# Kernel tuning notes

Hardware: AMD Instinct MI355X
Metric: run time of the kernel (lower is better)

Reference implementation:

```python
import jax, jax.numpy as jnp
import numpy as np

EPS = 1e-5

def conv2x2(x, w, b):
    # x: NCHW, w: OIHW (2x2), stride 2, valid padding
    y = jax.lax.conv_general_dilated(x, w, window_strides=(2, 2), padding='VALID',
                                     dimension_numbers=('NCHW', 'OIHW', 'NCHW'))
    return y + b[None, :, None, None]

def instancenorm(x):
    # per-sample, per-channel norm over H,W; biased variance, no affine (PyTorch defaults)
    mu = jnp.mean(x, axis=(2, 3), keepdims=True)
    var = jnp.mean(jnp.square(x - mu), axis=(2, 3), keepdims=True)
    return (x - mu) * jax.lax.rsqrt(var + EPS)

def lrelu(x):
    return jax.nn.leaky_relu(x, negative_slope=0.01)

def setup_inputs() -> dict:
    key = jax.random.key(0)
    ks = jax.random.split(key, 14)
    B, L = 256, 20
    s = 0.05
    inp = {
        'x': jax.random.normal(ks[0], (B, 3, 128, 128), jnp.float32),
        'labels': jax.random.uniform(ks[1], (B, L), jnp.float32),
        'w1': jax.random.normal(ks[2], (16, 3, 2, 2), jnp.float32) * s,
        'b1': jnp.zeros((16,), jnp.float32),
        'w2': jax.random.normal(ks[3], (32, 16 + L, 2, 2), jnp.float32) * s,
        'b2': jnp.zeros((32,), jnp.float32),
        'w3': jax.random.normal(ks[4], (64, 32, 2, 2), jnp.float32) * s,
        'b3': jnp.zeros((64,), jnp.float32),
        'w4': jax.random.normal(ks[5], (128, 64, 2, 2), jnp.float32) * s,
        'b4': jnp.zeros((128,), jnp.float32),
        'fcw1': jax.random.normal(ks[6], (1024, 128 * 8 * 8), jnp.float32) * s,
        'fcb1': jnp.zeros((1024,), jnp.float32),
        'fcw2': jax.random.normal(ks[7], (1, 1024), jnp.float32) * s,
        'fcb2': jnp.zeros((1,), jnp.float32),
    }
    return inp

def reference(x, labels, w1, b1, w2, b2, w3, b3, w4, b4, fcw1, fcb1, fcw2, fcb2):
    h = lrelu(instancenorm(conv2x2(x, w1, b1)))            # [B,16,64,64]
    # vectorized replacement of the per-element label broadcast loop
    lab = jnp.broadcast_to(labels[:, :, None, None],
                           (h.shape[0], labels.shape[1], h.shape[2], h.shape[3]))
    h = jnp.concatenate([h, lab], axis=1)                  # [B,36,64,64]
    h = lrelu(instancenorm(conv2x2(h, w2, b2)))            # [B,32,32,32]
    h = lrelu(instancenorm(conv2x2(h, w3, b3)))            # [B,64,16,16]
    h = lrelu(instancenorm(conv2x2(h, w4, b4)))            # [B,128,8,8]
    h = h.reshape(h.shape[0], -1)                          # [B,8192]
    h = lrelu(h @ fcw1.T + fcb1)                           # [B,1024]
    return h @ fcw2.T + fcb2                               # [B,1]
```

## Files before the change

kernel.cpp:

```cpp
#include <hip/hip_runtime.h>

#define EPSI 1e-5f

typedef __attribute__((ext_vector_type(8))) short bf16x8;
typedef __attribute__((ext_vector_type(4))) float f32x4;

__device__ __forceinline__ float lrelu(float x) { return x > 0.f ? x : 0.01f * x; }

__device__ __forceinline__ unsigned short f2bf(float x) {
    unsigned int u = __float_as_uint(x);
    return (unsigned short)((u + 0x7fffu + ((u >> 16) & 1u)) >> 16);
}
__device__ __forceinline__ float bflo(unsigned int v) { return __uint_as_float(v << 16); }
__device__ __forceinline__ float bfhi(unsigned int v) { return __uint_as_float(v & 0xFFFF0000u); }
__device__ __forceinline__ unsigned int pack2(float a, float b) {
    return (unsigned int)f2bf(a) | ((unsigned int)f2bf(b) << 16);
}
__device__ __forceinline__ bf16x8 pack8(float4 a, float4 b) {
    union { unsigned short u[8]; bf16x8 v; } p;
    p.u[0] = f2bf(a.x); p.u[1] = f2bf(a.y); p.u[2] = f2bf(a.z); p.u[3] = f2bf(a.w);
    p.u[4] = f2bf(b.x); p.u[5] = f2bf(b.y); p.u[6] = f2bf(b.z); p.u[7] = f2bf(b.w);
    return p.v;
}

__device__ __forceinline__ float2 block_reduce_sum2(float a, float b) {
    #pragma unroll
    for (int off = 1; off < 64; off <<= 1) {
        a += __shfl_xor(a, off, 64);
        b += __shfl_xor(b, off, 64);
    }
    __shared__ float lds[8];
    const int t = threadIdx.x;
    if ((t & 63) == 0) { lds[2 * (t >> 6)] = a; lds[2 * (t >> 6) + 1] = b; }
    __syncthreads();
    a = lds[0] + lds[2] + lds[4] + lds[6];
    b = lds[1] + lds[3] + lds[5] + lds[7];
    return make_float2(a, b);
}


__global__ __launch_bounds__(1024) void wprep(const float* __restrict__ w2,
                                              const float* __restrict__ w3,
                                              const float* __restrict__ w4,
                                              unsigned short* __restrict__ wk) {
    const int g = blockIdx.x * 1024 + threadIdx.x;
    if (g < 2048) {
        const int co = g >> 6, k = g & 63;
        const int ic = (k >> 4) * 4 + (k & 3), row = (k >> 3) & 1, tx = (k >> 2) & 1;
        wk[g] = f2bf(w2[co * 144 + ic * 4 + row * 2 + tx]);
    } else if (g < 10240) {
        const int e = g - 2048, co = e >> 7, k = e & 127;
        const int ic = (k >> 4) * 4 + (k & 3), row = (k >> 3) & 1, tx = (k >> 2) & 1;
        wk[g] = f2bf(w3[co * 128 + ic * 4 + row * 2 + tx]);
    } else if (g < 43008) {
        const int e = g - 10240, co = e >> 8, k = e & 255;
        const int ic = (k >> 4) * 4 + (k & 3), row = (k >> 3) & 1, tx = (k >> 2) & 1;
        wk[g] = f2bf(w4[co * 256 + ic * 4 + row * 2 + tx]);
    }
}

__global__ __launch_bounds__(1024, 1) void k1234(const float* __restrict__ x,
                                                 const float* __restrict__ w1,
                                                 const unsigned short* __restrict__ wk,
                                                 unsigned short* __restrict__ h4) {
    const int n = blockIdx.x;
    const int t = threadIdx.x;
    const int w = t >> 6, l = t & 63;
    __shared__ __align__(16) unsigned char smem[131072];
    __shared__ float red[16][64][2];
    __shared__ float msc[64][2];
    unsigned short* h1s = (unsigned short*)smem;
    unsigned short* h2s = (unsigned short*)smem;
    unsigned short* h3s = (unsigned short*)(smem + 65536);
    float* ps = (float*)smem;

    {
        const float* xn = x + (size_t)n * 49152;
        float acc[16][4];
        #pragma unroll
        for (int j = 0; j < 16; ++j)
            #pragma unroll
            for (int q = 0; q < 4; ++q) acc[j][q] = 0.f;
        #pragma unroll 1
        for (int ic = 0; ic < 3; ++ic) {
            const float* p = xn + ic * 16384;
            float2 v0[4], v1[4];
            #pragma unroll
            for (int q = 0; q < 4; ++q) {
                const int idx = t + 1024 * q;
                const int oy = idx >> 6, ox = idx & 63;
                v0[q] = ((const float2*)(p + (2 * oy) * 128))[ox];
                v1[q] = ((const float2*)(p + (2 * oy + 1) * 128))[ox];
            }
            #pragma unroll
            for (int j = 0; j < 16; ++j) {
                const float4 wv = *(const float4*)(w1 + j * 12 + ic * 4);
                #pragma unroll
                for (int q = 0; q < 4; ++q)
                    acc[j][q] += v0[q].x * wv.x + v0[q].y * wv.y + v1[q].x * wv.z + v1[q].y * wv.w;
            }
        }
        #pragma unroll
        for (int j = 0; j < 16; ++j) {
            float s1 = acc[j][0] + acc[j][1] + acc[j][2] + acc[j][3];
            float s2 = acc[j][0] * acc[j][0] + acc[j][1] * acc[j][1] +
                       acc[j][2] * acc[j][2] + acc[j][3] * acc[j][3];
            #pragma unroll
            for (int off = 1; off < 64; off <<= 1) {
                s1 += __shfl_xor(s1, off, 64);
                s2 += __shfl_xor(s2, off, 64);
            }
            if (l == 0) { red[w][j][0] = s1; red[w][j][1] = s2; }
        }
        __syncthreads();
        if (t < 16) {
            float s1 = 0.f, s2 = 0.f;
            #pragma unroll
            for (int ww = 0; ww < 16; ++ww) { s1 += red[ww][t][0]; s2 += red[ww][t][1]; }
            const float mean = s1 * (1.f / 4096.f);
            const float var = s2 * (1.f / 4096.f) - mean * mean;
            msc[t][0] = mean; msc[t][1] = rsqrtf(var + EPSI);
        }
        __syncthreads();
        #pragma unroll
        for (int q = 0; q < 4; ++q) {
            const int px = t + 1024 * q;
            #pragma unroll
            for (int q4 = 0; q4 < 4; ++q4) {
                const float n0 = lrelu((acc[4 * q4 + 0][q] - msc[4 * q4 + 0][0]) * msc[4 * q4 + 0][1]);
                const float n1 = lrelu((acc[4 * q4 + 1][q] - msc[4 * q4 + 1][0]) * msc[4 * q4 + 1][1]);
                const float n2 = lrelu((acc[4 * q4 + 2][q] - msc[4 * q4 + 2][0]) * msc[4 * q4 + 2][1]);
                const float n3 = lrelu((acc[4 * q4 + 3][q] - msc[4 * q4 + 3][0]) * msc[4 * q4 + 3][1]);
                uint2 u; u.x = pack2(n0, n1); u.y = pack2(n2, n3);
                *(uint2*)(&h1s[((size_t)q4 * 4096 + px) * 4]) = u;
            }
        }
    }
    __syncthreads();

    {
        const unsigned short* wk2 = wk;
        bf16x8 af[2][2];
        #pragma unroll
        for (int cf = 0; cf < 2; ++cf)
            #pragma unroll
            for (int ks = 0; ks < 2; ++ks)
                af[cf][ks] = *(const bf16x8*)(wk2 + (cf * 16 + (l & 15)) * 64 + ks * 32 + (l >> 4) * 8);
        f32x4 acc[4][2];
        const f32x4 z = {0.f, 0.f, 0.f, 0.f};
        #pragma unroll
        for (int pg = 0; pg < 4; ++pg) { acc[pg][0] = z; acc[pg][1] = z; }
        const int row = (l >> 4) & 1, icq0 = (l >> 4) >> 1;
        #pragma unroll
        for (int pg = 0; pg < 4; ++pg) {
            const int oy = 2 * w + (pg >> 1);
            const int ox = (pg & 1) * 16 + (l & 15);
            #pragma unroll
            for (int ks = 0; ks < 2; ++ks) {
                const bf16x8 bv = *(const bf16x8*)(&h1s[(ks * 2 + icq0) * 16384 + (2 * oy + row) * 256 + ox * 8]);
                acc[pg][0] = __builtin_amdgcn_mfma_f32_16x16x32_bf16(af[0][ks], bv, acc[pg][0], 0, 0, 0);
                acc[pg][1] = __builtin_amdgcn_mfma_f32_16x16x32_bf16(af[1][ks], bv, acc[pg][1], 0, 0, 0);
            }
        }
        #pragma unroll
        for (int cf = 0; cf < 2; ++cf) {
            #pragma unroll
            for (int r = 0; r < 4; ++r) {
                float s1 = acc[0][cf][r] + acc[1][cf][r] + acc[2][cf][r] + acc[3][cf][r];
                float s2 = acc[0][cf][r] * acc[0][cf][r] + acc[1][cf][r] * acc[1][cf][r] +
                           acc[2][cf][r] * acc[2][cf][r] + acc[3][cf][r] * acc[3][cf][r];
                #pragma unroll
                for (int off = 1; off < 16; off <<= 1) {
                    s1 += __shfl_xor(s1, off, 64);
                    s2 += __shfl_xor(s2, off, 64);
                }
                if ((l & 15) == 0) {
                    red[w][cf * 16 + (l >> 4) * 4 + r][0] = s1;
                    red[w][cf * 16 + (l >> 4) * 4 + r][1] = s2;
                }
            }
        }
        __syncthreads();
        if (t < 32) {
            float s1 = 0.f, s2 = 0.f;
            #pragma unroll
            for (int ww = 0; ww < 16; ++ww) { s1 += red[ww][t][0]; s2 += red[ww][t][1]; }
            const float mean = s1 * (1.f / 1024.f);
            const float var = s2 * (1.f / 1024.f) - mean * mean;
            msc[t][0] = mean; msc[t][1] = rsqrtf(var + EPSI);
        }
        __syncthreads();
        #pragma unroll
        for (int pg = 0; pg < 4; ++pg) {
            const int px = w * 64 + pg * 16 + (l & 15);
            #pragma unroll
            for (int cf = 0; cf < 2; ++cf) {
                const int co0 = cf * 16 + (l >> 4) * 4;
                float v[4];
                #pragma unroll
                for (int r = 0; r < 4; ++r)
                    v[r] = lrelu((acc[pg][cf][r] - msc[co0 + r][0]) * msc[co0 + r][1]);
                uint2 u; u.x = pack2(v[0], v[1]); u.y = pack2(v[2], v[3]);
                *(uint2*)(&h2s[((cf * 4 + (l >> 4)) * 1024 + px) * 4]) = u;
            }
        }
    }
    __syncthreads();

    {
        const unsigned short* wk3 = wk + 2048;
        f32x4 acc[4];
        const f32x4 z = {0.f, 0.f, 0.f, 0.f};
        #pragma unroll
        for (int cf = 0; cf < 4; ++cf) acc[cf] = z;
        const int row = (l >> 4) & 1, icq0 = (l >> 4) >> 1;
        #pragma unroll
        for (int ks = 0; ks < 4; ++ks) {
            const bf16x8 bv = *(const bf16x8*)(&h2s[(ks * 2 + icq0) * 4096 + (2 * w + row) * 128 + (l & 15) * 8]);
            #pragma unroll
            for (int cf = 0; cf < 4; ++cf) {
                const bf16x8 af = *(const bf16x8*)(wk3 + (cf * 16 + (l & 15)) * 128 + ks * 32 + (l >> 4) * 8);
                acc[cf] = __builtin_amdgcn_mfma_f32_16x16x32_bf16(af, bv, acc[cf], 0, 0, 0);
            }
        }
        #pragma unroll
        for (int cf = 0; cf < 4; ++cf) {
            #pragma unroll
            for (int r = 0; r < 4; ++r) {
                float s1 = acc[cf][r], s2 = acc[cf][r] * acc[cf][r];
                #pragma unroll
                for (int off = 1; off < 16; off <<= 1) {
                    s1 += __shfl_xor(s1, off, 64);
                    s2 += __shfl_xor(s2, off, 64);
                }
                if ((l & 15) == 0) {
                    red[w][cf * 16 + (l >> 4) * 4 + r][0] = s1;
                    red[w][cf * 16 + (l >> 4) * 4 + r][1] = s2;
                }
            }
        }
        __syncthreads();
        if (t < 64) {
            float s1 = 0.f, s2 = 0.f;
            #pragma unroll
            for (int ww = 0; ww < 16; ++ww) { s1 += red[ww][t][0]; s2 += red[ww][t][1]; }
            const float mean = s1 * (1.f / 256.f);
            const float var = s2 * (1.f / 256.f) - mean * mean;
            msc[t][0] = mean; msc[t][1] = rsqrtf(var + EPSI);
        }
        __syncthreads();
        const int px = w * 16 + (l & 15);
        #pragma unroll
        for (int cf = 0; cf < 4; ++cf) {
            const int co0 = cf * 16 + (l >> 4) * 4;
            float v[4];
            #pragma unroll
            for (int r = 0; r < 4; ++r)
                v[r] = lrelu((acc[cf][r] - msc[co0 + r][0]) * msc[co0 + r][1]);
            uint2 u; u.x = pack2(v[0], v[1]); u.y = pack2(v[2], v[3]);
            *(uint2*)(&h3s[((cf * 4 + (l >> 4)) * 256 + px) * 4]) = u;
        }
    }
    __syncthreads();

    {
        const unsigned short* wk4 = wk + 10240;
        const int cfp = w & 3, khalf = (w >> 2) & 1;
        f32x4 acc[4][2];
        const f32x4 z = {0.f, 0.f, 0.f, 0.f};
        #pragma unroll
        for (int pg = 0; pg < 4; ++pg) { acc[pg][0] = z; acc[pg][1] = z; }
        const int row = (l >> 4) & 1, icq0 = (l >> 4) >> 1;
        const int oyb = (l & 15) >> 3, ox = l & 7;
        if (w < 8) {
            #pragma unroll
            for (int ksl = 0; ksl < 4; ++ksl) {
                const int ks = khalf * 4 + ksl;
                bf16x8 af0 = *(const bf16x8*)(wk4 + ((cfp * 2 + 0) * 16 + (l & 15)) * 256 + ks * 32 + (l >> 4) * 8);
                bf16x8 af1 = *(const bf16x8*)(wk4 + ((cfp * 2 + 1) * 16 + (l & 15)) * 256 + ks * 32 + (l >> 4) * 8);
                #pragma unroll
                for (int pg = 0; pg < 4; ++pg) {
                    const int oy = pg * 2 + oyb;
                    const bf16x8 bv = *(const bf16x8*)(&h3s[(ks * 2 + icq0) * 1024 + (2 * oy + row) * 64 + ox * 8]);
                    acc[pg][0] = __builtin_amdgcn_mfma_f32_16x16x32_bf16(af0, bv, acc[pg][0], 0, 0, 0);
                    acc[pg][1] = __builtin_amdgcn_mfma_f32_16x16x32_bf16(af1, bv, acc[pg][1], 0, 0, 0);
                }
            }
        }
        if (w < 4) {
            #pragma unroll
            for (int pg = 0; pg < 4; ++pg)
                #pragma unroll
                for (int cfi = 0; cfi < 2; ++cfi)
                    #pragma unroll
                    for (int r = 0; r < 4; ++r)
                        ps[(cfp * 64 + l) * 32 + pg * 8 + cfi * 4 + r] = acc[pg][cfi][r];
        }
        __syncthreads();
        if (w >= 4 && w < 8) {
            unsigned short* on = h4 + (size_t)n * 8192;
            #pragma unroll
            for (int cfi = 0; cfi < 2; ++cfi) {
                #pragma unroll
                for (int r = 0; r < 4; ++r) {
                    float v[4];
                    #pragma unroll
                    for (int pg = 0; pg < 4; ++pg)
                        v[pg] = acc[pg][cfi][r] + ps[(cfp * 64 + l) * 32 + pg * 8 + cfi * 4 + r];
                    float s1 = v[0] + v[1] + v[2] + v[3];
                    float s2 = v[0] * v[0] + v[1] * v[1] + v[2] * v[2] + v[3] * v[3];
                    #pragma unroll
                    for (int off = 1; off < 16; off <<= 1) {
                        s1 += __shfl_xor(s1, off, 64);
                        s2 += __shfl_xor(s2, off, 64);
                    }
                    const float mean = s1 * (1.f / 64.f);
                    const float var = s2 * (1.f / 64.f) - mean * mean;
                    const float sc = rsqrtf(var + EPSI);
                    const int co = (cfp * 2 + cfi) * 16 + (l >> 4) * 4 + r;
                    #pragma unroll
                    for (int pg = 0; pg < 4; ++pg)
                        on[co * 64 + pg * 16 + (l & 15)] = f2bf(lrelu((v[pg] - mean) * sc));
                }
            }
        }
    }
}

__global__ __launch_bounds__(256, 2) void k5_fc1(const unsigned short* __restrict__ A,
                                                 const float* __restrict__ Wf,
                                                 unsigned short* __restrict__ Cp) {
    __shared__ unsigned short As[128 * 72];
    __shared__ unsigned short Bs[128 * 72];
    const int t = threadIdx.x;
    const int sk = blockIdx.x >> 4;
    const int tile = blockIdx.x & 15;
    const int mt = tile >> 3, nt = tile & 7;
    const int m0 = mt * 128, n0 = nt * 128;
    const int w = t >> 6, l = t & 63;
    const int wm = (w >> 1) * 64, wn = (w & 1) * 64;
    const int lr16 = l & 15, lk8 = (l >> 4) * 8;
    const int srow = t >> 3, scol = (t & 7) * 8;
    f32x4 acc[4][4];
    const f32x4 z = {0.f, 0.f, 0.f, 0.f};
    #pragma unroll
    for (int f = 0; f < 4; ++f)
        #pragma unroll
        for (int g = 0; g < 4; ++g) acc[f][g] = z;
    const int kbeg = sk * 256;
    #pragma unroll 1
    for (int kt = 0; kt < 4; ++kt) {
        const int kc = kbeg + kt * 64;
        bf16x8 av[4], bv[4];
        #pragma unroll
        for (int i = 0; i < 4; ++i) {
            av[i] = *(const bf16x8*)(A + (size_t)(m0 + srow + 32 * i) * 8192 + kc + scol);
            const float4 w0 = *(const float4*)(Wf + (size_t)(n0 + srow + 32 * i) * 8192 + kc + scol);
            const float4 w1 = *(const float4*)(Wf + (size_t)(n0 + srow + 32 * i) * 8192 + kc + scol + 4);
            bv[i] = pack8(w0, w1);
        }
        __syncthreads();
        #pragma unroll
        for (int i = 0; i < 4; ++i) {
            *(bf16x8*)&As[(srow + 32 * i) * 72 + scol] = av[i];
            *(bf16x8*)&Bs[(srow + 32 * i) * 72 + scol] = bv[i];
        }
        __syncthreads();
        #pragma unroll
        for (int ks = 0; ks < 2; ++ks) {
            bf16x8 af[4], bfr[4];
            #pragma unroll
            for (int f = 0; f < 4; ++f)
                af[f] = *(const bf16x8*)&As[(wm + f * 16 + lr16) * 72 + ks * 32 + lk8];
            #pragma unroll
            for (int g = 0; g < 4; ++g)
                bfr[g] = *(const bf16x8*)&Bs[(wn + g * 16 + lr16) * 72 + ks * 32 + lk8];
            #pragma unroll
            for (int f = 0; f < 4; ++f)
                #pragma unroll
                for (int g = 0; g < 4; ++g)
                    acc[f][g] = __builtin_amdgcn_mfma_f32_16x16x32_bf16(af[f], bfr[g], acc[f][g], 0, 0, 0);
        }
    }
    const int orow = (l >> 4) * 4, ocol = l & 15;
    #pragma unroll
    for (int f = 0; f < 4; ++f) {
        #pragma unroll
        for (int g = 0; g < 4; ++g) {
            #pragma unroll
            for (int j = 0; j < 4; ++j) {
                const int m = m0 + wm + f * 16 + orow + j;
                const int nn = n0 + wn + g * 16 + ocol;
                Cp[((size_t)sk * 256 + m) * 1024 + nn] = f2bf(acc[f][g][j]);
            }
        }
    }
}

__global__ __launch_bounds__(256) void k6_fc2(const unsigned short* __restrict__ Cp,
                                              const float* __restrict__ bias,
                                              const float* __restrict__ w,
                                              const float* __restrict__ b,
                                              float* __restrict__ out) {
    const int n = blockIdx.x, t = threadIdx.x;
    const int nn0 = t * 4;
    float s0 = 0.f, s1 = 0.f, s2 = 0.f, s3 = 0.f;
    #pragma unroll
    for (int sk = 0; sk < 32; ++sk) {
        const uint2 u = *(const uint2*)(Cp + ((size_t)sk * 256 + n) * 1024 + nn0);
        s0 += bflo(u.x); s1 += bfhi(u.x); s2 += bflo(u.y); s3 += bfhi(u.y);
    }
    const float4 bi = *(const float4*)(bias + nn0);
    const float4 wv = *(const float4*)(w + nn0);
    float part = lrelu(s0 + bi.x) * wv.x + lrelu(s1 + bi.y) * wv.y +
                 lrelu(s2 + bi.z) * wv.z + lrelu(s3 + bi.w) * wv.w;
    const float2 red = block_reduce_sum2(part, 0.f);
    if (t == 0) out[n] = red.x + b[0];
}

extern "C" void kernel_launch(void* const* d_in, const int* in_sizes, int n_in,
                              void* d_out, int out_size, void* d_ws, size_t ws_size,
                              hipStream_t stream) {
    (void)in_sizes; (void)n_in; (void)out_size; (void)ws_size;
    const float* x    = (const float*)d_in[0];
    const float* w1   = (const float*)d_in[2];
    const float* w2   = (const float*)d_in[4];
    const float* w3   = (const float*)d_in[6];
    const float* w4   = (const float*)d_in[8];
    const float* fcw1 = (const float*)d_in[10];
    const float* fcb1 = (const float*)d_in[11];
    const float* fcw2 = (const float*)d_in[12];
    const float* fcb2 = (const float*)d_in[13];
    float* out = (float*)d_out;
    float* bufA = (float*)d_ws;
    float* bufB = bufA + 16777216;
    unsigned short* h4 = (unsigned short*)bufB;
    unsigned short* wk = (unsigned short*)bufB + 12582912;
    unsigned short* Cp = (unsigned short*)bufA;
    wprep<<<42, 1024, 0, stream>>>(w2, w3, w4, wk);
    k1234<<<256, 1024, 0, stream>>>(x, w1, wk, h4);
    k5_fc1<<<512, 256, 0, stream>>>(h4, fcw1, Cp);
    k6_fc2<<<256, 256, 0, stream>>>(Cp, fcb1, fcw2, fcb2, out);
}
```

Before: 74.78 us.

## Split conv1 into two channel passes with float4 loads; use all 16 waves for conv4

Conv1 now runs as two passes of 8 output channels each. Each thread loads float4 input rows, covering two adjacent output pixels, and writes 16-byte packed bf16 stores. This lowers register pressure and widens memory accesses. Conv4 splits the K dimension four ways so all 16 waves issue MFMAs instead of 8, then combines the partial sums through two shared-memory buffers in a tree reduction. The cost is extra barriers and shared-memory traffic, and the h1s layout changes to channel-quad-major with adjacent pixel pairs, which stage 2 must still read correctly.

Result: slower. 86.97 us (+16.3%).

```diff
diff --git a/kernel.cpp b/kernel.cpp
--- a/kernel.cpp
+++ b/kernel.cpp
@@ -72,71 +72,91 @@
     unsigned short* h1s = (unsigned short*)smem;
     unsigned short* h2s = (unsigned short*)smem;
     unsigned short* h3s = (unsigned short*)(smem + 65536);
-    float* ps = (float*)smem;
+    float* psA = (float*)smem;
+    float* psB = (float*)(smem + 32768);
 
     {
         const float* xn = x + (size_t)n * 49152;
-        float acc[16][4];
-        #pragma unroll
-        for (int j = 0; j < 16; ++j)
-            #pragma unroll
-            for (int q = 0; q < 4; ++q) acc[j][q] = 0.f;
         #pragma unroll 1
-        for (int ic = 0; ic < 3; ++ic) {
-            const float* p = xn + ic * 16384;
-            float2 v0[4], v1[4];
-            #pragma unroll
-            for (int q = 0; q < 4; ++q) {
-                const int idx = t + 1024 * q;
-                const int oy = idx >> 6, ox = idx & 63;
-                v0[q] = ((const float2*)(p + (2 * oy) * 128))[ox];
-                v1[q] = ((const float2*)(p + (2 * oy + 1) * 128))[ox];
-            }
-            #pragma unroll
-            for (int j = 0; j < 16; ++j) {
-                const float4 wv = *(const float4*)(w1 + j * 12 + ic * 4);
-                #pragma unroll
-                for (int q = 0; q < 4; ++q)
-                    acc[j][q] += v0[q].x * wv.x + v0[q].y * wv.y + v1[q].x * wv.z + v1[q].y * wv.w;
-            }
-        }
-        #pragma unroll
-        for (int j = 0; j < 16; ++j) {
-            float s1 = acc[j][0] + acc[j][1] + acc[j][2] + acc[j][3];
-            float s2 = acc[j][0] * acc[j][0] + acc[j][1] * acc[j][1] +
-                       acc[j][2] * acc[j][2] + acc[j][3] * acc[j][3];
-            #pragma unroll
-            for (int off = 1; off < 64; off <<= 1) {
-                s1 += __shfl_xor(s1, off, 64);
-                s2 += __shfl_xor(s2, off, 64);
-            }
-            if (l == 0) { red[w][j][0] = s1; red[w][j][1] = s2; }
-        }
-        __syncthreads();
-        if (t < 16) {
-            float s1 = 0.f, s2 = 0.f;
-            #pragma unroll
-            for (int ww = 0; ww < 16; ++ww) { s1 += red[ww][t][0]; s2 += red[ww][t][1]; }
-            const float mean = s1 * (1.f / 4096.f);
-            const float var = s2 * (1.f / 4096.f) - mean * mean;
-            msc[t][0] = mean; msc[t][1] = rsqrtf(var + EPSI);
-        }
-        __syncthreads();
-        #pragma unroll
-        for (int q = 0; q < 4; ++q) {
-            const int px = t + 1024 * q;
-            #pragma unroll
-            for (int q4 = 0; q4 < 4; ++q4) {
-                const float n0 = lrelu((acc[4 * q4 + 0][q] - msc[4 * q4 + 0][0]) * msc[4 * q4 + 0][1]);
-                const float n1 = lrelu((acc[4 * q4 + 1][q] - msc[4 * q4 + 1][0]) * msc[4 * q4 + 1][1]);
-                const float n2 = lrelu((acc[4 * q4 + 2][q] - msc[4 * q4 + 2][0]) * msc[4 * q4 + 2][1]);
-                const float n3 = lrelu((acc[4 * q4 + 3][q] - msc[4 * q4 + 3][0]) * msc[4 * q4 + 3][1]);
-                uint2 u; u.x = pack2(n0, n1); u.y = pack2(n2, n3);
-                *(uint2*)(&h1s[((size_t)q4 * 4096 + px) * 4]) = u;
-            }
-        }
-    }
-    __syncthreads();
+        for (int pass = 0; pass < 2; ++pass) {
+            float acc[8][4];
+            #pragma unroll
+            for (int j = 0; j < 8; ++j)
+                #pragma unroll
+                for (int q = 0; q < 4; ++q) acc[j][q] = 0.f;
+            float4 r0[2][3], r1[2][3];
+            #pragma unroll
+            for (int qq = 0; qq < 2; ++qq) {
+                const int p = t + 1024 * qq;
+                const int oy = p >> 5;
+                const int ox0 = (2 * p) & 63;
+                #pragma unroll
+                for (int ic = 0; ic < 3; ++ic) {
+                    r0[qq][ic] = *(const float4*)(xn + ic * 16384 + (2 * oy) * 128 + 2 * ox0);
+                    r1[qq][ic] = *(const float4*)(xn + ic * 16384 + (2 * oy + 1) * 128 + 2 * ox0);
+                }
+            }
+            #pragma unroll
+            for (int j = 0; j < 8; ++j) {
+                #pragma unroll
+                for (int ic = 0; ic < 3; ++ic) {
+                    const float4 wv = *(const float4*)(w1 + (pass * 8 + j) * 12 + ic * 4);
+                    #pragma unroll
+                    for (int qq = 0; qq < 2; ++qq) {
+                        acc[j][qq * 2 + 0] += r0[qq][ic].x * wv.x + r0[qq][ic].y * wv.y +
+                                              r1[qq][ic].x * wv.z + r1[qq][ic].y * wv.w;
+                        acc[j][qq * 2 + 1] += r0[qq][ic].z * wv.x + r0[qq][ic].w * wv.y +
+                                              r1[qq][ic].z * wv.z + r1[qq][ic].w * wv.w;
+                    }
+                }
+            }
+            #pragma unroll
+            for (int j = 0; j < 8; ++j) {
+                float s1 = acc[j][0] + acc[j][1] + acc[j][2] + acc[j][3];
+                float s2 = acc[j][0] * acc[j][0] + acc[j][1] * acc[j][1] +
+                           acc[j][2] * acc[j][2] + acc[j][3] * acc[j][3];
+                #pragma unroll
+                for (int off = 1; off < 64; off <<= 1) {
+                    s1 += __shfl_xor(s1, off, 64);
+                    s2 += __shfl_xor(s2, off, 64);
+                }
+                if (l == 0) { red[w][j][0] = s1; red[w][j][1] = s2; }
+            }
+            __syncthreads();
+            if (t < 8) {
+                float s1 = 0.f, s2 = 0.f;
+                #pragma unroll
+                for (int ww = 0; ww < 16; ++ww) { s1 += red[ww][t][0]; s2 += red[ww][t][1]; }
+                const float mean = s1 * (1.f / 4096.f);
+                const float var = s2 * (1.f / 4096.f) - mean * mean;
+                msc[t][0] = mean; msc[t][1] = rsqrtf(var + EPSI);
+            }
+            __syncthreads();
+            #pragma unroll
+            for (int qq = 0; qq < 2; ++qq) {
+                const int p = t + 1024 * qq;
+                const int oy = p >> 5;
+                const int ox0 = (2 * p) & 63;
+                const int base = (oy * 64 + ox0) * 4;
+                #pragma unroll
+                for (int c4 = 0; c4 < 2; ++c4) {
+                    const int icq = pass * 2 + c4;
+                    float ns[2][4];
+                    #pragma unroll
+                    for (int s = 0; s < 2; ++s)
+                        #pragma unroll
+                        for (int c = 0; c < 4; ++c)
+                            ns[s][c] = lrelu((acc[c4 * 4 + c][qq * 2 + s] - msc[c4 * 4 + c][0]) *
+                                             msc[c4 * 4 + c][1]);
+                    uint4 u;
+                    u.x = pack2(ns[0][0], ns[0][1]); u.y = pack2(ns[0][2], ns[0][3]);
+                    u.z = pack2(ns[1][0], ns[1][1]); u.w = pack2(ns[1][2], ns[1][3]);
+                    *(uint4*)(&h1s[icq * 16384 + base]) = u;
+                }
+            }
+            __syncthreads();
+        }
+    }
 
     {
         const unsigned short* wk2 = wk;
@@ -265,39 +285,59 @@
 
     {
         const unsigned short* wk4 = wk + 10240;
-        const int cfp = w & 3, khalf = (w >> 2) & 1;
+        const int cfp = w & 3, kq = w >> 2;
         f32x4 acc[4][2];
         const f32x4 z = {0.f, 0.f, 0.f, 0.f};
         #pragma unroll
         for (int pg = 0; pg < 4; ++pg) { acc[pg][0] = z; acc[pg][1] = z; }
         const int row = (l >> 4) & 1, icq0 = (l >> 4) >> 1;
         const int oyb = (l & 15) >> 3, ox = l & 7;
-        if (w < 8) {
-            #pragma unroll
-            for (int ksl = 0; ksl < 4; ++ksl) {
-                const int ks = khalf * 4 + ksl;
-                bf16x8 af0 = *(const bf16x8*)(wk4 + ((cfp * 2 + 0) * 16 + (l & 15)) * 256 + ks * 32 + (l >> 4) * 8);
-                bf16x8 af1 = *(const bf16x8*)(wk4 + ((cfp * 2 + 1) * 16 + (l & 15)) * 256 + ks * 32 + (l >> 4) * 8);
-                #pragma unroll
-                for (int pg = 0; pg < 4; ++pg) {
-                    const int oy = pg * 2 + oyb;
-                    const bf16x8 bv = *(const bf16x8*)(&h3s[(ks * 2 + icq0) * 1024 + (2 * oy + row) * 64 + ox * 8]);
-                    acc[pg][0] = __builtin_amdgcn_mfma_f32_16x16x32_bf16(af0, bv, acc[pg][0], 0, 0, 0);
-                    acc[pg][1] = __builtin_amdgcn_mfma_f32_16x16x32_bf16(af1, bv, acc[pg][1], 0, 0, 0);
-                }
-            }
-        }
-        if (w < 4) {
+        #pragma unroll
+        for (int ksl = 0; ksl < 2; ++ksl) {
+            const int ks = kq * 2 + ksl;
+            bf16x8 af0 = *(const bf16x8*)(wk4 + ((cfp * 2 + 0) * 16 + (l & 15)) * 256 + ks * 32 + (l >> 4) * 8);
+            bf16x8 af1 = *(const bf16x8*)(wk4 + ((cfp * 2 + 1) * 16 + (l & 15)) * 256 + ks * 32 + (l >> 4) * 8);
+            #pragma unroll
+            for (int pg = 0; pg < 4; ++pg) {
+                const int oy = pg * 2 + oyb;
+                const bf16x8 bv = *(const bf16x8*)(&h3s[(ks * 2 + icq0) * 1024 + (2 * oy + row) * 64 + ox * 8]);
+                acc[pg][0] = __builtin_amdgcn_mfma_f32_16x16x32_bf16(af0, bv, acc[pg][0], 0, 0, 0);
+                acc[pg][1] = __builtin_amdgcn_mfma_f32_16x16x32_bf16(af1, bv, acc[pg][1], 0, 0, 0);
+            }
+        }
+        const int pbase = (cfp * 64 + l) * 32;
+        if (kq == 1 || kq == 3) {
+            float* dst = (kq == 1) ? psA : psB;
             #pragma unroll
             for (int pg = 0; pg < 4; ++pg)
                 #pragma unroll
                 for (int cfi = 0; cfi < 2; ++cfi)
                     #pragma unroll
                     for (int r = 0; r < 4; ++r)
-                        ps[(cfp * 64 + l) * 32 + pg * 8 + cfi * 4 + r] = acc[pg][cfi][r];
-        }
-        __syncthreads();
-        if (w >= 4 && w < 8) {
+                        dst[pbase + pg * 8 + cfi * 4 + r] = acc[pg][cfi][r];
+        }
+        __syncthreads();
+        if (kq == 0) {
+            #pragma unroll
+            for (int pg = 0; pg < 4; ++pg)
+                #pragma unroll
+                for (int cfi = 0; cfi < 2; ++cfi)
+                    #pragma unroll
+                    for (int r = 0; r < 4; ++r)
+                        acc[pg][cfi][r] += psA[pbase + pg * 8 + cfi * 4 + r];
+        } else if (kq == 2) {
+            #pragma unroll
+            for (int pg = 0; pg < 4; ++pg)
+                #pragma unroll
+                for (int cfi = 0; cfi < 2; ++cfi)
+                    #pragma unroll
+                    for (int r = 0; r < 4; ++r) {
+                        acc[pg][cfi][r] += psB[pbase + pg * 8 + cfi * 4 + r];
+                        psB[pbase + pg * 8 + cfi * 4 + r] = acc[pg][cfi][r];
+                    }
+        }
+        __syncthreads();
+        if (kq == 0) {
             unsigned short* on = h4 + (size_t)n * 8192;
             #pragma unroll
             for (int cfi = 0; cfi < 2; ++cfi) {
@@ -306,7 +346,7 @@
                     float v[4];
                     #pragma unroll
                     for (int pg = 0; pg < 4; ++pg)
-                        v[pg] = acc[pg][cfi][r] + ps[(cfp * 64 + l) * 32 + pg * 8 + cfi * 4 + r];
+                        v[pg] = acc[pg][cfi][r] + psB[pbase + pg * 8 + cfi * 4 + r];
                     float s1 = v[0] + v[1] + v[2] + v[3];
                     float s2 = v[0] * v[0] + v[1] * v[1] + v[2] * v[2] + v[3] * v[3];
                     #pragma unroll
```
